# Kernel tuning notes

Measured on AMD Instinct MI355X. Metric: run time of the kernel, lower is better.

Reference implementation:

```python
import jax, jax.numpy as jnp
import numpy as np

# dims: batch, points, patches(groups), patch size, hidden, heads, layers, ffn
B, N, G, K, D, H, L, F = 32, 8192, 256, 32, 384, 6, 12, 1536
MASK_RATIO = 0.75
LEN_KEEP = int(G * (1 - MASK_RATIO))  # 64 visible tokens
HD = D // H


def _layernorm(x, g, b, eps=1e-5):
    m = jnp.mean(x, -1, keepdims=True)
    v = jnp.mean(jnp.square(x - m), -1, keepdims=True)
    return (x - m) * jax.lax.rsqrt(v + eps) * g + b


def _normalize_points(x):
    # normalize(): center = mid of bbox, radius = max distance to center (iso/diag)
    bmin = x.min(-2, keepdims=True)
    bmax = x.max(-2, keepdims=True)
    center = 0.5 * (bmin + bmax)
    radius = jnp.linalg.norm(x - center, axis=-1, keepdims=True).max(-2, keepdims=True)
    return (x - center) / radius


def _fps(x, num_samples):
    # farthest point sampling; sequential by nature -> fori_loop over G (fixed, small)
    b, n, _ = x.shape
    idxs = jnp.zeros((b, num_samples), jnp.int32)

    def body(i, state):
        dists, idxs, last = state
        lastpt = jnp.take_along_axis(x, last[:, None, None].astype(jnp.int32), axis=1)  # [B,1,3]
        d = jnp.sum(jnp.square(x - lastpt), -1)  # [B,N]
        dists = jnp.minimum(dists, d)
        nxt = jnp.argmax(dists, -1).astype(jnp.int32)
        return dists, idxs.at[:, i].set(nxt), nxt

    dists0 = jnp.full((b, n), 1e10, x.dtype)
    _, idxs, _ = jax.lax.fori_loop(1, num_samples, body, (dists0, idxs, jnp.zeros((b,), jnp.int32)))
    return idxs


def _group(x, centers):
    # squared pairwise distances without materializing [B,G,N,3]
    d2 = (jnp.sum(jnp.square(centers), -1)[:, :, None]
          + jnp.sum(jnp.square(x), -1)[:, None, :]
          - 2.0 * jnp.einsum('bgc,bnc->bgn', centers, x))  # [B,G,N]
    _, idx = jax.lax.top_k(-d2, K)  # [B,G,K] knn indices
    nbrs = jnp.take_along_axis(x[:, None, :, :], idx[..., None], axis=2)  # [B,G,K,3] (_knn_gather)
    return nbrs - centers[:, :, None, :]


def setup_inputs() -> dict:
    key = jax.random.key(0)
    ks = iter(jax.random.split(key, 24))

    def w(shape, scale=0.02):
        return jax.random.normal(next(ks), shape, jnp.float32) * scale

    ones_ln = jnp.stack([jnp.ones(D, jnp.float32), jnp.zeros(D, jnp.float32)])
    return {
        'points': jax.random.normal(next(ks), (B, N, 3), jnp.float32),
        'noise': jax.random.uniform(next(ks), (B, G), jnp.float32),
        # mini-PointNet patch encoder
        'pe_w1': w((3, 128)), 'pe_b1': jnp.zeros((128,), jnp.float32),
        'pe_w2': w((128, 256)), 'pe_b2': jnp.zeros((256,), jnp.float32),
        'pe_w3': w((256, D)), 'pe_b3': jnp.zeros((D,), jnp.float32),
        # positional MLP on patch centers
        'pos_w1': w((3, 128)), 'pos_b1': jnp.zeros((128,), jnp.float32),
        'pos_w2': w((128, D)), 'pos_b2': jnp.zeros((D,), jnp.float32),
        # transformer (stacked over L layers)
        'ln1': jnp.tile(ones_ln[None], (L, 1, 1)),
        'wqkv': w((L, D, 3 * D)), 'bqkv': jnp.zeros((L, 3 * D), jnp.float32),
        'wo': w((L, D, D)), 'bo': jnp.zeros((L, D), jnp.float32),
        'ln2': jnp.tile(ones_ln[None], (L, 1, 1)),
        'wi': w((L, D, F)), 'bi': jnp.zeros((L, F), jnp.float32),
        'wo2': w((L, F, D)), 'bo2': jnp.zeros((L, D), jnp.float32),
        'lnf': ones_ln,
    }


def _forward(points, noise, pe_w1, pe_b1, pe_w2, pe_b2, pe_w3, pe_b3,
             pos_w1, pos_b1, pos_w2, pos_b2,
             ln1, wqkv, bqkv, wo, bo, ln2, wi, bi, wo2, bo2, lnf):
    x = _normalize_points(points)
    cidx = _fps(x, G)                                        # [B,G]
    centers = jnp.take_along_axis(x, cidx[..., None], axis=1)  # [B,G,3]
    patches = _group(x, centers)                              # [B,G,K,3]

    # patch encode (per-point MLP -> max pool -> proj)
    f = jax.nn.relu(patches @ pe_w1 + pe_b1)
    f = f @ pe_w2 + pe_b2
    tokens = f.max(axis=2) @ pe_w3 + pe_b3                    # [B,G,D]
    pos = jax.nn.relu(centers @ pos_w1 + pos_b1) @ pos_w2 + pos_b2  # [B,G,D]

    # mask(): argsort-of-noise shuffle, keep first len_keep tokens
    ids_shuffle = jnp.argsort(noise, axis=1)
    ids_keep = ids_shuffle[:, :LEN_KEEP]                      # [B,64]
    h = (jnp.take_along_axis(tokens, ids_keep[..., None], axis=1)
         + jnp.take_along_axis(pos, ids_keep[..., None], axis=1))  # [B,64,D]

    scale = 1.0 / jnp.sqrt(jnp.asarray(HD, h.dtype))

    def layer(h, p):
        l1, wq, bq, wo_, bo_, l2, wi_, bi_, wo2_, bo2_ = p
        y = _layernorm(h, l1[0], l1[1])
        qkv = (y @ wq + bq).reshape(B, LEN_KEEP, 3, H, HD)  # '(three h d)' split
        q, k, v = jnp.moveaxis(qkv, 2, 0)
        a = jax.nn.softmax(jnp.einsum('bshd,bthd->bhst', q, k) * scale, -1)
        o = jnp.einsum('bhst,bthd->bshd', a, v).reshape(B, LEN_KEEP, D)
        h = h + o @ wo_ + bo_
        y = _layernorm(h, l2[0], l2[1])
        h = h + jax.nn.gelu(y @ wi_ + bi_) @ wo2_ + bo2_
        return h, None

    h, _ = jax.lax.scan(layer, h, (ln1, wqkv, bqkv, wo, bo, ln2, wi, bi, wo2, bo2))
    return _layernorm(h, lnf[0], lnf[1])


def reference(points, noise, pe_w1, pe_b1, pe_w2, pe_b2, pe_w3, pe_b3,
              pos_w1, pos_b1, pos_w2, pos_b2,
              ln1, wqkv, bqkv, wo, bo, ln2, wi, bi, wo2, bo2, lnf):
    return _forward(points, noise, pe_w1, pe_b1, pe_w2, pe_b2, pe_w3, pe_b3,
                    pos_w1, pos_b1, pos_w2, pos_b2,
                    ln1, wqkv, bqkv, wo, bo, ln2, wi, bi, wo2, bo2, lnf)
```

## Files before the change

kernel.cpp:

```cpp
#include <hip/hip_runtime.h>

#define NPTS 8192
#define NB   32
#define NG   256
#define NK   32
#define ND   384
#define NH   6
#define NLK  64
#define NF   1536
#define NHD  64
#define NL   12
#define MM   2048

typedef unsigned short u16;
typedef unsigned long long u64;
typedef __attribute__((ext_vector_type(8))) short short8;
typedef __attribute__((ext_vector_type(16))) float f32x16;
typedef __attribute__((ext_vector_type(4))) unsigned short ushort4v;

#define PL_PRE   147456ull
#define PL_LAYER 1769472ull
#define WT_ELEMS (PL_PRE + 12ull*PL_LAYER)

__device__ __forceinline__ float bf2f(u16 v){
  unsigned int u = ((unsigned int)v) << 16;
  float f; __builtin_memcpy(&f, &u, 4); return f;
}
__device__ __forceinline__ float ldf(const void* p, size_t i, bool bf){
  if(bf) return bf2f(((const u16*)p)[i]);
  return ((const float*)p)[i];
}
__device__ __forceinline__ u16 f2bf(float f){
  unsigned int x; __builtin_memcpy(&x, &f, 4);
  x += 0x7fffu + ((x >> 16) & 1u);
  return (u16)(x >> 16);
}
__device__ __forceinline__ void split2(float v, u16& hi, u16& lo){
  hi = f2bf(v);
  lo = f2bf(v - bf2f(hi));
}

__device__ __forceinline__ float blockMax256(float v, float* sb, int tid){
  for(int off=32; off; off>>=1) v = fmaxf(v, __shfl_down(v, off));
  __syncthreads();
  if((tid&63)==0) sb[tid>>6] = v;
  __syncthreads();
  return fmaxf(fmaxf(sb[0],sb[1]), fmaxf(sb[2],sb[3]));
}

__global__ __launch_bounds__(256) void k_normalize(const void* __restrict__ pts,
                                                   float* __restrict__ xn,
                                                   int* __restrict__ flag){
#pragma clang fp contract(off)
  int b = blockIdx.x, tid = threadIdx.x;
  __shared__ float sb[4];
  __shared__ int sbad;
  if(tid==0) sbad = 0;
  __syncthreads();
  {
    const u16* p16 = (const u16*)pts;
    int hit=0;
    for(int i=tid; i<4096; i+=256){
      unsigned e = (p16[i] >> 7) & 0xFFu;
      if(e >= 0x90u) hit=1;
    }
    if(hit) atomicOr(&sbad, 1);
  }
  __syncthreads();
  const bool bf = (sbad == 0);
  if(b==0 && tid==0) flag[0] = bf ? 1 : 0;
  const size_t base = (size_t)b*NPTS*3;
  float mn0=1e30f,mn1=1e30f,mn2=1e30f, mx0=-1e30f,mx1=-1e30f,mx2=-1e30f;
  for(int n=tid; n<NPTS; n+=256){
    float x0=ldf(pts,base+n*3,bf), x1=ldf(pts,base+n*3+1,bf), x2=ldf(pts,base+n*3+2,bf);
    mn0=fminf(mn0,x0); mx0=fmaxf(mx0,x0);
    mn1=fminf(mn1,x1); mx1=fmaxf(mx1,x1);
    mn2=fminf(mn2,x2); mx2=fmaxf(mx2,x2);
  }
  mx0=blockMax256(mx0,sb,tid); mn0=-blockMax256(-mn0,sb,tid);
  mx1=blockMax256(mx1,sb,tid); mn1=-blockMax256(-mn1,sb,tid);
  mx2=blockMax256(mx2,sb,tid); mn2=-blockMax256(-mn2,sb,tid);
  float c0=0.5f*(mn0+mx0), c1=0.5f*(mn1+mx1), c2=0.5f*(mn2+mx2);
  float mr=0.0f;
  for(int n=tid; n<NPTS; n+=256){
    float d0=ldf(pts,base+n*3,bf)-c0, d1=ldf(pts,base+n*3+1,bf)-c1, d2=ldf(pts,base+n*3+2,bf)-c2;
    float nr = sqrtf((d0*d0 + d1*d1) + d2*d2);
    mr = fmaxf(mr, nr);
  }
  float radius = blockMax256(mr, sb, tid);
  float* XO = xn + base;
  for(int n=tid; n<NPTS; n+=256){
    XO[n*3  ] = (ldf(pts,base+n*3  ,bf)-c0)/radius;
    XO[n*3+1] = (ldf(pts,base+n*3+1,bf)-c1)/radius;
    XO[n*3+2] = (ldf(pts,base+n*3+2,bf)-c2)/radius;
  }
}

__device__ __forceinline__ void kmax_dpp_step(unsigned& hi, unsigned& lo, unsigned oh, unsigned ol){
  bool g = (oh > hi) || (oh == hi && ol > lo);
  hi = g ? oh : hi; lo = g ? ol : lo;
}
#define KMAX_DPP(CTRL) { \
  unsigned oh=(unsigned)__builtin_amdgcn_update_dpp(0,(int)kh,(CTRL),0xf,0xf,true); \
  unsigned ol=(unsigned)__builtin_amdgcn_update_dpp(0,(int)kl,(CTRL),0xf,0xf,true); \
  kmax_dpp_step(kh,kl,oh,ol); }

__global__ __launch_bounds__(512) void k_fps_trans(
    const float* __restrict__ xn, float* __restrict__ centers,
    const void* __restrict__ noise, int* __restrict__ keep,
    const void* __restrict__ pe_w3, const void* __restrict__ pos_w2,
    const void* __restrict__ wqkv, const void* __restrict__ wo,
    const void* __restrict__ wi,   const void* __restrict__ wo2,
    u16* __restrict__ wthi, u16* __restrict__ wtlo,
    const int* __restrict__ flag)
{
  __shared__ float xs[NPTS*3];
  __shared__ u64 skey[3];
  __shared__ int sc[NG];
  int tid = threadIdx.x;

  if(blockIdx.x >= 64){
    const bool bf = flag[0]!=0;
    float (*t)[33] = reinterpret_cast<float(*)[33]>(xs);
    int gid = blockIdx.x - 64;
    const void* W; int Kd, Nd; size_t woff, doff; int local;
    if(gid < 96){        W=pe_w3;  Kd=256; Nd=384; woff=0; doff=0;      local=gid; }
    else if(gid < 144){  W=pos_w2; Kd=128; Nd=384; woff=0; doff=98304;  local=gid-96; }
    else{
      int g2 = gid - 144; int l = g2 / 1728; int id = g2 % 1728;
      size_t lb = PL_PRE + (size_t)l*PL_LAYER;
      if(id < 432){        W=wqkv; Kd=384;  Nd=1152; woff=(size_t)l*442368; doff=lb;          local=id; }
      else if(id < 576){   W=wo;   Kd=384;  Nd=384;  woff=(size_t)l*147456; doff=lb+442368;   local=id-432; }
      else if(id < 1152){  W=wi;   Kd=384;  Nd=1536; woff=(size_t)l*589824; doff=lb+589824;   local=id-576; }
      else {               W=wo2;  Kd=1536; Nd=384;  woff=(size_t)l*589824; doff=lb+1179648;  local=id-1152; }
    }
    int ntiles = Nd >> 5;
    int n0 = (local % ntiles)*32, k0 = (local / ntiles)*32;
    for(int i=0;i<2;i++){
      int idx = tid + i*512; int kr = idx>>5, nc = idx&31;
      t[kr][nc] = ldf(W, woff + (size_t)(k0+kr)*Nd + n0+nc, bf);
    }
    __syncthreads();
    for(int i=0;i<2;i++){
      int idx = tid + i*512; int nr = idx>>5, kc = idx&31;
      float v = t[kc][nr];
      u16 hi,lo; split2(v,hi,lo);
      size_t o = doff + (size_t)(n0+nr)*Kd + k0+kc;
      wthi[o]=hi; wtlo[o]=lo;
    }
    return;
  }

  if(blockIdx.x >= 32){
    const bool bf = flag[0]!=0;
    int b = blockIdx.x - 32;
    float* nv = xs;
    if(tid < NG) nv[tid] = ldf(noise, (size_t)b*NG+tid, bf);
    __syncthreads();
    if(tid < NG){
      float v = nv[tid]; int r = 0;
      for(int j=0; j<NG; j++){
        float u = nv[j];
        r += (u < v) || (u == v && j < tid);
      }
      if(r < NLK) keep[b*NLK + r] = tid;
    }
    return;
  }

  {
#pragma clang fp contract(off)
    int b = blockIdx.x;
    int lane = tid & 63;
    const float* X = xn + (size_t)b*NPTS*3;
    float px[16],py[16],pz[16],dd[16];
#pragma unroll
    for(int s=0;s<16;s++){
      int n = s*512 + tid;
      px[s]=X[n*3]; py[s]=X[n*3+1]; pz[s]=X[n*3+2];
      dd[s]=1e10f;
    }
    for(int i=tid; i<NPTS*3; i+=512) xs[i] = X[i];
    if(tid==0){ skey[0]=0ull; skey[1]=0ull; skey[2]=0ull; sc[0]=0; }
    __syncthreads();
    float lx = xs[0], ly = xs[1], lz = xs[2];
    for(int i=1;i<NG;i++){
      int c = i % 3;
      float bv=-1.0f; int bs=0;
#pragma unroll
      for(int s=0;s<16;s++){
        float dx=px[s]-lx, dy=py[s]-ly, dz=pz[s]-lz;
        float d=(dx*dx + dy*dy) + dz*dz;
        d = fminf(dd[s], d); dd[s]=d;
        if(d > bv){ bv=d; bs=s; }
      }
      int bn = bs*512 + tid;
      unsigned kh; __builtin_memcpy(&kh,&bv,4);
      unsigned kl = (unsigned)(NPTS-1-bn);
      KMAX_DPP(0x111)
      KMAX_DPP(0x112)
      KMAX_DPP(0x114)
      KMAX_DPP(0x118)
      KMAX_DPP(0x142)
      KMAX_DPP(0x143)
      if(lane==63) atomicMax(&skey[c], ((u64)kh<<32) | (u64)kl);
      __syncthreads();
      u64 k64 = skey[c];
      int n = (NPTS-1) - (int)(k64 & 0xFFFFFFFFull);
      n &= (NPTS-1);
      if(tid==0){ sc[i]=n; skey[(i+2)%3]=0ull; }
      lx = xs[n*3]; ly = xs[n*3+1]; lz = xs[n*3+2];
    }
    __syncthreads();
    if(tid < NG){
      int n = sc[tid] & (NPTS-1);
      centers[((size_t)b*NG+tid)*3  ] = xs[n*3];
      centers[((size_t)b*NG+tid)*3+1] = xs[n*3+1];
      centers[((size_t)b*NG+tid)*3+2] = xs[n*3+2];
    }
  }
}

__global__ __launch_bounds__(256) void k_knn(
    const float* __restrict__ xn, const float* __restrict__ centers,
    const int* __restrict__ keep, float* __restrict__ patches)
{
  int blk=blockIdx.x; int b=blk>>6; int j=blk&63; int tid=threadIdx.x;
  __shared__ float sd[NPTS];
  __shared__ int   sel[NK];
  __shared__ float rv[4]; __shared__ int rn[4];
  __shared__ int   sseln;
  int g = keep[b*NLK + j] & (NG-1);
  const float* C = centers + ((size_t)b*NG + g)*3;
  float c0=C[0], c1=C[1], c2=C[2];
  const float* X = xn + (size_t)b*NPTS*3;
  {
#pragma clang fp contract(off)
    float cc = (c0*c0 + c1*c1) + c2*c2;
    for(int n=tid; n<NPTS; n+=256){
      float x0=X[n*3], x1=X[n*3+1], x2=X[n*3+2];
      float xx=(x0*x0 + x1*x1) + x2*x2;
      float dt=(c0*x0 + c1*x1) + c2*x2;
      sd[n] = (cc + xx) - 2.0f*dt;
    }
  }
  __syncthreads();
  float dl[32];
  for(int s=0;s<32;s++) dl[s] = sd[s*256 + tid];
  unsigned int alive = 0xffffffffu;
  for(int r=0; r<NK; r++){
    float bv=1e30f; int bn=0x7fffffff;
    for(int s=0;s<32;s++){
      if(alive & (1u<<s)){
        float v = dl[s];
        if(v < bv){ bv=v; bn=s*256+tid; }
      }
    }
    for(int off=32;off;off>>=1){
      float ov=__shfl_down(bv,off); int on=__shfl_down(bn,off);
      if(ov<bv || (ov==bv && on<bn)){ bv=ov; bn=on; }
    }
    if((tid&63)==0){ rv[tid>>6]=bv; rn[tid>>6]=bn; }
    __syncthreads();
    if(tid==0){
      float v=rv[0]; int n=rn[0];
      for(int w=1;w<4;w++) if(rv[w]<v || (rv[w]==v && rn[w]<n)){ v=rv[w]; n=rn[w]; }
      n &= (NPTS-1);
      sseln=n; sel[r]=n;
    }
    __syncthreads();
    int n = sseln;
    if((n & 255) == tid) alive &= ~(1u << (n >> 8));
  }
  __syncthreads();
  if(tid < NK){
    int n = sel[tid] & (NPTS-1);
    float* P = patches + ((size_t)(b*NLK+j)*NK + tid)*3;
    P[0]=X[n*3  ]-c0;
    P[1]=X[n*3+1]-c1;
    P[2]=X[n*3+2]-c2;
  }
}

__global__ __launch_bounds__(256) void k_embed(
    const float* __restrict__ patches, const float* __restrict__ centers,
    const int* __restrict__ keep,
    const void* __restrict__ w1, const void* __restrict__ b1,
    const void* __restrict__ w2, const void* __restrict__ b2,
    const void* __restrict__ pw1, const void* __restrict__ pb1,
    u16* __restrict__ mfhi, u16* __restrict__ mflo,
    u16* __restrict__ phhi, u16* __restrict__ phlo,
    const int* __restrict__ flag)
{
  int blk=blockIdx.x; int b=blk>>6; int j=blk&63; int tid=threadIdx.x;
  const bool bf = flag[0] != 0;
  __shared__ float pat[NK*3];
  __shared__ __align__(16) float f1t[128*36];
  int row = b*NLK + j;
  if(tid < NK*3) pat[tid] = patches[(size_t)row*NK*3 + tid];
  __syncthreads();
  for(int i=0;i<16;i++){
    int idx = tid + i*256;
    int k = idx>>7, m = idx&127;
    float v = ldf(b1,m,bf)
            + pat[k*3+0]*ldf(w1,        m,bf)
            + pat[k*3+1]*ldf(w1, 128 + m,bf)
            + pat[k*3+2]*ldf(w1, 256 + m,bf);
    f1t[m*36 + k] = fmaxf(v, 0.0f);
  }
  __syncthreads();
  float acc[NK];
  {
    float bv = ldf(b2, tid, bf);
#pragma unroll
    for(int k=0;k<NK;k++) acc[k]=bv;
  }
  for(int jj=0;jj<128;jj++){
    float wv = ldf(w2, (size_t)jj*256+tid, bf);
    const float* fr = &f1t[jj*36];
#pragma unroll
    for(int k8=0;k8<8;k8++){
      float4 fv = *reinterpret_cast<const float4*>(fr + k8*4);
      acc[k8*4+0] = fmaf(fv.x, wv, acc[k8*4+0]);
      acc[k8*4+1] = fmaf(fv.y, wv, acc[k8*4+1]);
      acc[k8*4+2] = fmaf(fv.z, wv, acc[k8*4+2]);
      acc[k8*4+3] = fmaf(fv.w, wv, acc[k8*4+3]);
    }
  }
  float mx = acc[0];
#pragma unroll
  for(int k=1;k<NK;k++) mx = fmaxf(mx, acc[k]);
  { u16 hi,lo; split2(mx,hi,lo);
    mfhi[(size_t)row*256 + tid]=hi; mflo[(size_t)row*256 + tid]=lo; }
  if(tid < 128){
    int g = keep[b*NLK + j] & (NG-1);
    const float* C = centers + ((size_t)b*NG + g)*3;
    float v = ldf(pb1,tid,bf)
            + C[0]*ldf(pw1,        tid,bf)
            + C[1]*ldf(pw1, 128 + tid,bf)
            + C[2]*ldf(pw1, 256 + tid,bf);
    v = fmaxf(v, 0.0f);
    u16 hi,lo; split2(v,hi,lo);
    phhi[(size_t)row*128 + tid]=hi; phlo[(size_t)row*128 + tid]=lo;
  }
}

__global__ __launch_bounds__(256) void k_transpose4(
    const void* __restrict__ wqkv, const void* __restrict__ wo,
    const void* __restrict__ wi,   const void* __restrict__ wo2,
    int l, u16* __restrict__ dhi, u16* __restrict__ dlo,
    const int* __restrict__ flag){
  __shared__ float t[32][33];
  const bool bf = flag[0]!=0;
  int id = blockIdx.x;
  const void* W; int Kd, Nd; size_t woff, doff; int local;
  if(id < 432){        W=wqkv; Kd=384;  Nd=1152; woff=(size_t)l*442368; doff=PL_PRE;          local=id; }
  else if(id < 576){   W=wo;   Kd=384;  Nd=384;  woff=(size_t)l*147456; doff=PL_PRE+442368;   local=id-432; }
  else if(id < 1152){  W=wi;   Kd=384;  Nd=1536; woff=(size_t)l*589824; doff=PL_PRE+589824;   local=id-576; }
  else {               W=wo2;  Kd=1536; Nd=384;  woff=(size_t)l*589824; doff=PL_PRE+1179648;  local=id-1152; }
  int ntiles = Nd >> 5;
  int n0 = (local % ntiles)*32, k0 = (local / ntiles)*32;
  for(int i=0;i<4;i++){
    int idx = threadIdx.x + i*256; int kr = idx>>5, nc = idx&31;
    t[kr][nc] = ldf(W, woff + (size_t)(k0+kr)*Nd + n0+nc, bf);
  }
  __syncthreads();
  for(int i=0;i<4;i++){
    int idx = threadIdx.x + i*256; int nr = idx>>5, kc = idx&31;
    float v = t[kc][nr];
    u16 hi,lo; split2(v,hi,lo);
    size_t o = doff + (size_t)(n0+nr)*Kd + k0+kc;
    dhi[o]=hi; dlo[o]=lo;
  }
}

__global__ __launch_bounds__(128) void k_ln_split(const float* __restrict__ X,
                                                  const void* __restrict__ gb, size_t go,
                                                  u16* __restrict__ Yhi, u16* __restrict__ Ylo,
                                                  const int* __restrict__ flag){
  int row=blockIdx.x, tid=threadIdx.x;
  const bool bf = flag[0] != 0;
  const float* x = X + (size_t)row*ND;
  __shared__ float sbuf[2];
  float v0=x[tid], v1=x[tid+128], v2=x[tid+256];
  float s = v0+v1+v2;
  for(int off=32;off;off>>=1) s += __shfl_down(s,off);
  if((tid&63)==0) sbuf[tid>>6]=s;
  __syncthreads();
  float mean = (sbuf[0]+sbuf[1]) * (1.0f/(float)ND);
  __syncthreads();
  float d0=v0-mean, d1=v1-mean, d2=v2-mean;
  s = d0*d0 + d1*d1 + d2*d2;
  for(int off=32;off;off>>=1) s += __shfl_down(s,off);
  if((tid&63)==0) sbuf[tid>>6]=s;
  __syncthreads();
  float var = (sbuf[0]+sbuf[1]) * (1.0f/(float)ND);
  float rstd = 1.0f / sqrtf(var + 1e-5f);
  float o0 = d0*rstd*ldf(gb,go+tid    ,bf) + ldf(gb,go+ND+tid    ,bf);
  float o1 = d1*rstd*ldf(gb,go+tid+128,bf) + ldf(gb,go+ND+tid+128,bf);
  float o2 = d2*rstd*ldf(gb,go+tid+256,bf) + ldf(gb,go+ND+tid+256,bf);
  u16 hi,lo; size_t rb = (size_t)row*ND;
  split2(o0,hi,lo); Yhi[rb+tid    ]=hi; Ylo[rb+tid    ]=lo;
  split2(o1,hi,lo); Yhi[rb+tid+128]=hi; Ylo[rb+tid+128]=lo;
  split2(o2,hi,lo); Yhi[rb+tid+256]=hi; Ylo[rb+tid+256]=lo;
}

template<int TM, int TN, int ACT, bool RES, bool OSPLIT>
__global__ __launch_bounds__(256) void k_gemm_mfma(
    const u16* __restrict__ Ahi, const u16* __restrict__ Alo,
    const u16* __restrict__ Whi, const u16* __restrict__ Wlo, size_t wo,
    const void* __restrict__ bias, size_t bo, const int* __restrict__ flag,
    const float* __restrict__ res, float* __restrict__ Cf,
    u16* __restrict__ Ohi, u16* __restrict__ Olo,
    int N, int K)
{
  __shared__ __align__(16) u16 sAh[2][64*40];
  __shared__ __align__(16) u16 sAl[2][64*40];
  __shared__ __align__(16) u16 sBh[2][64*40];
  __shared__ __align__(16) u16 sBl[2][64*40];
  int tid = threadIdx.x;
  int wave = tid >> 6, lane = tid & 63;
  int wm = wave >> 1, wn = wave & 1;
  int l31 = lane & 31, half = lane >> 5;
  int row0 = blockIdx.y*TM, col0 = blockIdx.x*TN;
  const bool bf = flag[0] != 0;
  f32x16 acc;
#pragma unroll
  for(int r=0;r<16;r++) acc[r]=0.f;

  const int sr  = tid >> 2;
  const int scc = (tid & 3) * 8;
  const u16* gAh = Ahi + (size_t)(row0+sr)*K + scc;
  const u16* gAl = Alo + (size_t)(row0+sr)*K + scc;
  const u16* gBh = Whi + wo + (size_t)(col0+sr)*K + scc;
  const u16* gBl = Wlo + wo + (size_t)(col0+sr)*K + scc;
  const int ldst = sr*40 + scc;

  uint4 rah = *reinterpret_cast<const uint4*>(gAh);
  uint4 ral = *reinterpret_cast<const uint4*>(gAl);
  uint4 rbh = *reinterpret_cast<const uint4*>(gBh);
  uint4 rbl = *reinterpret_cast<const uint4*>(gBl);

  const int nk = K >> 5;
  for(int t=0; t<nk; ++t){
    const int buf = t & 1;
    *reinterpret_cast<uint4*>(&sAh[buf][ldst]) = rah;
    *reinterpret_cast<uint4*>(&sAl[buf][ldst]) = ral;
    *reinterpret_cast<uint4*>(&sBh[buf][ldst]) = rbh;
    *reinterpret_cast<uint4*>(&sBl[buf][ldst]) = rbl;
    __syncthreads();
    if(t+1 < nk){
      const int ko = (t+1) << 5;
      rah = *reinterpret_cast<const uint4*>(gAh + ko);
      ral = *reinterpret_cast<const uint4*>(gAl + ko);
      rbh = *reinterpret_cast<const uint4*>(gBh + ko);
      rbl = *reinterpret_cast<const uint4*>(gBl + ko);
    }
#pragma unroll
    for(int ks=0; ks<2; ks++){
      int aoff = (wm*32 + l31)*40 + ks*16 + half*8;
      int boff = (wn*32 + l31)*40 + ks*16 + half*8;
      short8 ah = *reinterpret_cast<const short8*>(&sAh[buf][aoff]);
      short8 al = *reinterpret_cast<const short8*>(&sAl[buf][aoff]);
      short8 bh = *reinterpret_cast<const short8*>(&sBh[buf][boff]);
      short8 bl = *reinterpret_cast<const short8*>(&sBl[buf][boff]);
      acc = __builtin_amdgcn_mfma_f32_32x32x16_bf16(ah, bh, acc, 0,0,0);
      acc = __builtin_amdgcn_mfma_f32_32x32x16_bf16(ah, bl, acc, 0,0,0);
      acc = __builtin_amdgcn_mfma_f32_32x32x16_bf16(al, bh, acc, 0,0,0);
    }
  }
  int col = col0 + wn*32 + l31;
  float bv = ldf(bias, bo+col, bf);
#pragma unroll
  for(int r=0;r<16;r++){
    int row = row0 + wm*32 + (r&3) + 8*(r>>2) + 4*half;
    float v = acc[r] + bv;
    if(ACT==1){
      float xx = v;
      v = 0.5f*xx*(1.0f + tanhf(0.7978845608028654f*(xx + 0.044715f*xx*xx*xx)));
    }
    if(RES) v += res[(size_t)row*N + col];
    if(OSPLIT){
      u16 hi,lo; split2(v,hi,lo);
      Ohi[(size_t)row*N + col]=hi; Olo[(size_t)row*N + col]=lo;
    }else{
      Cf[(size_t)row*N + col]=v;
    }
  }
}

__global__ __launch_bounds__(256) void k_attn_pl(const float* __restrict__ qkv,
                                                 u16* __restrict__ ohi,
                                                 u16* __restrict__ olo){
  __shared__ float Qt[64*68];
  __shared__ float Kt[64*68];
  __shared__ float V [64*68];
  __shared__ float SB[64*68];
  int blk=blockIdx.x; int b=blk/NH, h=blk%NH;
  int tid=threadIdx.x;
  for(int idx=tid; idx<4096; idx+=256){
    int s=idx>>6, d=idx&63;
    const float* r = qkv + ((size_t)(b*NLK+s))*1152 + h*NHD + d;
    Qt[d*68+s]=r[0];
    Kt[d*68+s]=r[384];
    V [s*68+d]=r[768];
  }
  __syncthreads();
  {
    const int i0 = (tid>>4)*4, j0 = (tid&15)*4;
    float a00=0.f,a01=0.f,a02=0.f,a03=0.f;
    float a10=0.f,a11=0.f,a12=0.f,a13=0.f;
    float a20=0.f,a21=0.f,a22=0.f,a23=0.f;
    float a30=0.f,a31=0.f,a32=0.f,a33=0.f;
#pragma unroll 4
    for(int d=0;d<64;d++){
      float4 qa = *reinterpret_cast<const float4*>(&Qt[d*68+i0]);
      float4 kb = *reinterpret_cast<const float4*>(&Kt[d*68+j0]);
      a00=fmaf(qa.x,kb.x,a00); a01=fmaf(qa.x,kb.y,a01); a02=fmaf(qa.x,kb.z,a02); a03=fmaf(qa.x,kb.w,a03);
      a10=fmaf(qa.y,kb.x,a10); a11=fmaf(qa.y,kb.y,a11); a12=fmaf(qa.y,kb.z,a12); a13=fmaf(qa.y,kb.w,a13);
      a20=fmaf(qa.z,kb.x,a20); a21=fmaf(qa.z,kb.y,a21); a22=fmaf(qa.z,kb.z,a22); a23=fmaf(qa.z,kb.w,a23);
      a30=fmaf(qa.w,kb.x,a30); a31=fmaf(qa.w,kb.y,a31); a32=fmaf(qa.w,kb.z,a32); a33=fmaf(qa.w,kb.w,a33);
    }
    float4 o0 = {a00*0.125f, a01*0.125f, a02*0.125f, a03*0.125f};
    float4 o1 = {a10*0.125f, a11*0.125f, a12*0.125f, a13*0.125f};
    float4 o2 = {a20*0.125f, a21*0.125f, a22*0.125f, a23*0.125f};
    float4 o3 = {a30*0.125f, a31*0.125f, a32*0.125f, a33*0.125f};
    *reinterpret_cast<float4*>(&SB[(i0  )*68+j0]) = o0;
    *reinterpret_cast<float4*>(&SB[(i0+1)*68+j0]) = o1;
    *reinterpret_cast<float4*>(&SB[(i0+2)*68+j0]) = o2;
    *reinterpret_cast<float4*>(&SB[(i0+3)*68+j0]) = o3;
  }
  __syncthreads();
  if(tid<64){
    float* rowp=&SB[tid*68];
    float m=rowp[0];
    for(int j=1;j<64;j++) m=fmaxf(m,rowp[j]);
    float sum=0.0f;
    for(int j=0;j<64;j++){ float e=__expf(rowp[j]-m); rowp[j]=e; sum+=e; }
    for(int j=0;j<64;j++) Qt[j*68+tid] = rowp[j]/sum;
  }
  __syncthreads();
  {
    const int s0 = (tid>>4)*4, d0 = (tid&15)*4;
    float a00=0.f,a01=0.f,a02=0.f,a03=0.f;
    float a10=0.f,a11=0.f,a12=0.f,a13=0.f;
    float a20=0.f,a21=0.f,a22=0.f,a23=0.f;
    float a30=0.f,a31=0.f,a32=0.f,a33=0.f;
#pragma unroll 4
    for(int t=0;t<64;t++){
      float4 av = *reinterpret_cast<const float4*>(&Qt[t*68+s0]);
      float4 vv = *reinterpret_cast<const float4*>(&V [t*68+d0]);
      a00=fmaf(av.x,vv.x,a00); a01=fmaf(av.x,vv.y,a01); a02=fmaf(av.x,vv.z,a02); a03=fmaf(av.x,vv.w,a03);
      a10=fmaf(av.y,vv.x,a10); a11=fmaf(av.y,vv.y,a11); a12=fmaf(av.y,vv.z,a12); a13=fmaf(av.y,vv.w,a13);
      a20=fmaf(av.z,vv.x,a20); a21=fmaf(av.z,vv.y,a21); a22=fmaf(av.z,vv.z,a22); a23=fmaf(av.z,vv.w,a23);
      a30=fmaf(av.w,vv.x,a30); a31=fmaf(av.w,vv.y,a31); a32=fmaf(av.w,vv.z,a32); a33=fmaf(av.w,vv.w,a33);
    }
    float rr[4][4] = {{a00,a01,a02,a03},{a10,a11,a12,a13},{a20,a21,a22,a23},{a30,a31,a32,a33}};
#pragma unroll
    for(int si=0; si<4; si++){
      ushort4v h4, l4;
#pragma unroll
      for(int di=0; di<4; di++){
        u16 hi,lo; split2(rr[si][di],hi,lo);
        h4[di]=hi; l4[di]=lo;
      }
      size_t o = ((size_t)(b*NLK+s0+si))*ND + h*NHD + d0;
      *reinterpret_cast<ushort4v*>(&ohi[o]) = h4;
      *reinterpret_cast<ushort4v*>(&olo[o]) = l4;
    }
  }
}

template<bool FINAL>
__global__ __launch_bounds__(128) void k_ln(const float* __restrict__ X,
                                            const void* __restrict__ gb, size_t go,
                                            void* __restrict__ Y,
                                            const int* __restrict__ flag){
  int row=blockIdx.x, tid=threadIdx.x;
  const bool bf = flag[0] != 0;
  const float* x = X + (size_t)row*ND;
  __shared__ float sbuf[2];
  float v0=x[tid], v1=x[tid+128], v2=x[tid+256];
  float s = v0+v1+v2;
  for(int off=32;off;off>>=1) s += __shfl_down(s,off);
  if((tid&63)==0) sbuf[tid>>6]=s;
  __syncthreads();
  float mean = (sbuf[0]+sbuf[1]) * (1.0f/(float)ND);
  __syncthreads();
  float d0=v0-mean, d1=v1-mean, d2=v2-mean;
  s = d0*d0 + d1*d1 + d2*d2;
  for(int off=32;off;off>>=1) s += __shfl_down(s,off);
  if((tid&63)==0) sbuf[tid>>6]=s;
  __syncthreads();
  float var = (sbuf[0]+sbuf[1]) * (1.0f/(float)ND);
  float rstd = 1.0f / sqrtf(var + 1e-5f);
  float o0 = d0*rstd*ldf(gb,go+tid    ,bf) + ldf(gb,go+ND+tid    ,bf);
  float o1 = d1*rstd*ldf(gb,go+tid+128,bf) + ldf(gb,go+ND+tid+128,bf);
  float o2 = d2*rstd*ldf(gb,go+tid+256,bf) + ldf(gb,go+ND+tid+256,bf);
  if(FINAL && bf){
    u16* yo = (u16*)Y + (size_t)row*ND;
    yo[tid]=f2bf(o0); yo[tid+128]=f2bf(o1); yo[tid+256]=f2bf(o2);
  }else{
    float* yo = (float*)Y + (size_t)row*ND;
    yo[tid]=o0; yo[tid+128]=o1; yo[tid+256]=o2;
  }
}

extern "C" void kernel_launch(void* const* d_in, const int* in_sizes, int n_in,
                              void* d_out, int out_size, void* d_ws, size_t ws_size,
                              hipStream_t stream){
  (void)in_sizes; (void)n_in; (void)out_size;
  const void* pts   = d_in[0];
  const void* noise = d_in[1];
  const void* pe_w1 = d_in[2];
  const void* pe_b1 = d_in[3];
  const void* pe_w2 = d_in[4];
  const void* pe_b2 = d_in[5];
  const void* pe_w3 = d_in[6];
  const void* pe_b3 = d_in[7];
  const void* pos_w1= d_in[8];
  const void* pos_b1= d_in[9];
  const void* pos_w2= d_in[10];
  const void* pos_b2= d_in[11];
  const void* ln1   = d_in[12];
  const void* wqkv  = d_in[13];
  const void* bqkv  = d_in[14];
  const void* wo    = d_in[15];
  const void* bo    = d_in[16];
  const void* ln2   = d_in[17];
  const void* wi    = d_in[18];
  const void* bi    = d_in[19];
  const void* wo2   = d_in[20];
  const void* bo2   = d_in[21];
  const void* lnf   = d_in[22];

  const size_t needed_small = (6711296ull + 16) * 4;
  if (ws_size < needed_small) return;
  const size_t wt_f32_off = 6711312ull;
  const size_t needed_big = (wt_f32_off + WT_ELEMS) * 4;
  const bool big = ws_size >= needed_big;

  float* ws   = (float*)d_ws;
  float* h    = ws;
  u16*  yhi   = (u16*)(ws + 786432);
  u16*  ylo   = yhi + 786432;
  float* qkvb = ws + 1572864;
  u16*  athi  = (u16*)(ws + 3932160);
  u16*  atlo  = athi + 786432;
  u16*  ubhi  = (u16*)(ws + 1572864);
  u16*  ublo  = ubhi + 3145728;
  float* xn   = ws + 1572864;
  float* patches;
  float* centers;
  int*   keep;
  int*   flag;
  u16 *wthi, *wtlo;
  if(big){
    patches = ws + 6488064;
    centers = ws + 6684672;
    keep    = (int*)(ws + 6709248);
    flag    = (int*)(ws + 6711296);
    wthi    = (u16*)(ws + wt_f32_off);
    wtlo    = wthi + WT_ELEMS;
  }else{
    wthi    = (u16*)(ws + 4718592);
    wtlo    = (u16*)(ws + 5677056);
    patches = ws + 6635520;
    centers = ws + 6832128;
    keep    = (int*)(ws + 6856704);
    flag    = (int*)(ws + 6858752);
    if(ws_size < (6858752ull + 16) * 4) return;
  }

  k_normalize<<<NB, 256, 0, stream>>>(pts, xn, flag);
  {
    int grid = big ? (64 + 144 + 12*1728) : (64 + 144);
    k_fps_trans<<<grid, 512, 0, stream>>>(xn, centers, noise, keep, pe_w3, pos_w2,
        wqkv, wo, wi, wo2, wthi, wtlo, flag);
  }
  k_knn      <<<NB*NLK, 256, 0, stream>>>(xn, centers, keep, patches);
  k_embed    <<<NB*NLK, 256, 0, stream>>>(patches, centers, keep,
      pe_w1, pe_b1, pe_w2, pe_b2, pos_w1, pos_b1,
      yhi , yhi + 2048*256 , athi , athi + 2048*128 , flag);
  k_gemm_mfma<64,64,0,false,false><<<dim3(6,32), 256, 0, stream>>>(
      yhi, yhi + 2048*256, wthi, wtlo, 0, pe_b3, 0, flag, nullptr, h, nullptr, nullptr, 384, 256);
  k_gemm_mfma<64,64,0,true ,false><<<dim3(6,32), 256, 0, stream>>>(
      athi, athi + 2048*128, wthi, wtlo, 98304, pos_b2, 0, flag, h, h, nullptr, nullptr, 384, 128);

  for(int l=0; l<NL; l++){
    size_t lb = big ? (PL_PRE + (size_t)l*PL_LAYER) : PL_PRE;
    if(!big){
      k_transpose4<<<1728, 256, 0, stream>>>(wqkv, wo, wi, wo2, l, wthi, wtlo, flag);
    }
    k_ln_split<<<MM, 128, 0, stream>>>(h, ln1, (size_t)l*2*ND, yhi, ylo, flag);
    k_gemm_mfma<64,64,0,false,false><<<dim3(18,32), 256, 0, stream>>>(
        yhi, ylo, wthi, wtlo, lb, bqkv, (size_t)l*1152, flag, nullptr, qkvb, nullptr, nullptr, 1152, 384);
    k_attn_pl<<<NB*NH, 256, 0, stream>>>(qkvb, athi, atlo);
    k_gemm_mfma<64,64,0,true ,false><<<dim3(6,32), 256, 0, stream>>>(
        athi, atlo, wthi, wtlo, lb + 442368, bo, (size_t)l*384, flag, h, h, nullptr, nullptr, 384, 384);
    k_ln_split<<<MM, 128, 0, stream>>>(h, ln2, (size_t)l*2*ND, yhi, ylo, flag);
    k_gemm_mfma<64,64,1,false,true ><<<dim3(24,32), 256, 0, stream>>>(
        yhi, ylo, wthi, wtlo, lb + 589824, bi, (size_t)l*1536, flag, nullptr, nullptr, ubhi, ublo, 1536, 384);
    k_gemm_mfma<64,64,0,true ,false><<<dim3(6,32), 256, 0, stream>>>(
        ubhi, ublo, wthi, wtlo, lb + 1179648, bo2, (size_t)l*384, flag, h, h, nullptr, nullptr, 384, 1536);
  }
  k_ln<true><<<MM, 128, 0, stream>>>(h, lnf, 0, d_out, flag);
}
```

Before: 1.804 ms.

## Stage split-bf16 GEMM tiles with direct global-to-LDS loads and XOR swizzle

The MFMA GEMM no longer loads A/B hi/lo tiles into registers and then stores them to shared memory. It now uses global_load_lds to copy 16-byte chunks straight into the double-buffered LDS tiles, prefetching the next k-slice after the barrier. Because the direct-to-LDS layout is fixed per lane, the row padding (stride 40) is replaced by an XOR swizzle of 8-element chunks to avoid bank conflicts on the MFMA fragment reads. This cuts register pressure and VALU/LDS-store instructions in the main loop. It relies on the barrier also waiting for the outstanding LDS DMA, and on the swizzle being mirrored correctly on the read side.

```diff
diff --git a/kernel.cpp b/kernel.cpp
--- a/kernel.cpp
+++ b/kernel.cpp
@@ -38,6 +38,11 @@
 __device__ __forceinline__ void split2(float v, u16& hi, u16& lo){
   hi = f2bf(v);
   lo = f2bf(v - bf2f(hi));
+}
+__device__ __forceinline__ void gl_lds16(const u16* g, u16* l){
+  __builtin_amdgcn_global_load_lds(
+    (const __attribute__((address_space(1))) void*)g,
+    (__attribute__((address_space(3))) void*)l, 16, 0, 0);
 }
 
 __device__ __forceinline__ float blockMax256(float v, float* sb, int tid){
@@ -414,10 +419,10 @@
     u16* __restrict__ Ohi, u16* __restrict__ Olo,
     int N, int K)
 {
-  __shared__ __align__(16) u16 sAh[2][64*40];
-  __shared__ __align__(16) u16 sAl[2][64*40];
-  __shared__ __align__(16) u16 sBh[2][64*40];
-  __shared__ __align__(16) u16 sBl[2][64*40];
+  __shared__ __align__(16) u16 sAh[2][64*32];
+  __shared__ __align__(16) u16 sAl[2][64*32];
+  __shared__ __align__(16) u16 sBh[2][64*32];
+  __shared__ __align__(16) u16 sBl[2][64*32];
   int tid = threadIdx.x;
   int wave = tid >> 6, lane = tid & 63;
   int wm = wave >> 1, wn = wave & 1;
@@ -429,37 +434,37 @@
   for(int r=0;r<16;r++) acc[r]=0.f;
 
   const int sr  = tid >> 2;
-  const int scc = (tid & 3) * 8;
-  const u16* gAh = Ahi + (size_t)(row0+sr)*K + scc;
-  const u16* gAl = Alo + (size_t)(row0+sr)*K + scc;
-  const u16* gBh = Whi + wo + (size_t)(col0+sr)*K + scc;
-  const u16* gBl = Wlo + wo + (size_t)(col0+sr)*K + scc;
-  const int ldst = sr*40 + scc;
-
-  uint4 rah = *reinterpret_cast<const uint4*>(gAh);
-  uint4 ral = *reinterpret_cast<const uint4*>(gAl);
-  uint4 rbh = *reinterpret_cast<const uint4*>(gBh);
-  uint4 rbl = *reinterpret_cast<const uint4*>(gBl);
+  const int scs = ((tid & 3) ^ (sr & 3)) * 8;
+  const u16* gAh = Ahi + (size_t)(row0+sr)*K + scs;
+  const u16* gAl = Alo + (size_t)(row0+sr)*K + scs;
+  const u16* gBh = Whi + wo + (size_t)(col0+sr)*K + scs;
+  const u16* gBl = Wlo + wo + (size_t)(col0+sr)*K + scs;
+  const int ldst = tid*8;
 
   const int nk = K >> 5;
+  gl_lds16(gAh, &sAh[0][ldst]);
+  gl_lds16(gAl, &sAl[0][ldst]);
+  gl_lds16(gBh, &sBh[0][ldst]);
+  gl_lds16(gBl, &sBl[0][ldst]);
+
+  const int ra = wm*32 + l31, rb = wn*32 + l31;
+  const int rax = ra & 3,     rbx = rb & 3;
+
   for(int t=0; t<nk; ++t){
     const int buf = t & 1;
-    *reinterpret_cast<uint4*>(&sAh[buf][ldst]) = rah;
-    *reinterpret_cast<uint4*>(&sAl[buf][ldst]) = ral;
-    *reinterpret_cast<uint4*>(&sBh[buf][ldst]) = rbh;
-    *reinterpret_cast<uint4*>(&sBl[buf][ldst]) = rbl;
     __syncthreads();
     if(t+1 < nk){
       const int ko = (t+1) << 5;
-      rah = *reinterpret_cast<const uint4*>(gAh + ko);
-      ral = *reinterpret_cast<const uint4*>(gAl + ko);
-      rbh = *reinterpret_cast<const uint4*>(gBh + ko);
-      rbl = *reinterpret_cast<const uint4*>(gBl + ko);
+      gl_lds16(gAh + ko, &sAh[buf^1][ldst]);
+      gl_lds16(gAl + ko, &sAl[buf^1][ldst]);
+      gl_lds16(gBh + ko, &sBh[buf^1][ldst]);
+      gl_lds16(gBl + ko, &sBl[buf^1][ldst]);
     }
 #pragma unroll
     for(int ks=0; ks<2; ks++){
-      int aoff = (wm*32 + l31)*40 + ks*16 + half*8;
-      int boff = (wn*32 + l31)*40 + ks*16 + half*8;
+      int c16 = ks*2 + half;
+      int aoff = ra*32 + ((c16 ^ rax) << 3);
+      int boff = rb*32 + ((c16 ^ rbx) << 3);
       short8 ah = *reinterpret_cast<const short8*>(&sAh[buf][aoff]);
       short8 al = *reinterpret_cast<const short8*>(&sAl[buf][aoff]);
       short8 bh = *reinterpret_cast<const short8*>(&sBh[buf][boff]);
```

Measured after the change: 1.935 ms. +7.2%, slower.
